# Optimization experiments

Hardware: AMD Instinct MI355X
Metric: run time of the kernel (lower is better)

The kernel has to match this reference:

```python
import jax, jax.numpy as jnp
import numpy as np

N = 10000
IN_DIM = 256
HID = 256
HEADS = 8
NUM_CLASSES = 40
EPS = 1e-5
NEG_SLOPE = 0.2


def gat_conv(x, src, dst, W, a_src, a_dst, bias, concat):
    # x: [N, F_in]; W: [F_in, H*C]; a_src/a_dst: [H, C]
    n = x.shape[0]
    H, C = a_src.shape
    h = (x @ W).reshape(n, H, C)                       # [N,H,C]
    s_src = jnp.einsum('nhc,hc->nh', h, a_src)         # [N,H]
    s_dst = jnp.einsum('nhc,hc->nh', h, a_dst)         # [N,H]
    score = jax.nn.leaky_relu(s_src[src] + s_dst[dst], NEG_SLOPE)  # [E,H]
    m = jax.lax.stop_gradient(jax.ops.segment_max(score, dst, num_segments=n))
    e = jnp.exp(score - m[dst])                        # [E,H]
    denom = jax.ops.segment_sum(e, dst, num_segments=n)
    alpha = e / denom[dst]                             # per-dst edge softmax
    msg = h[src] * alpha[:, :, None]                   # [E,H,C]
    out = jax.ops.segment_sum(msg, dst, num_segments=n)  # [N,H,C]
    out = out.reshape(n, H * C) if concat else out.mean(axis=1)
    return out + bias


def batch_norm(x, gamma, beta):
    mu = x.mean(axis=0)
    var = x.var(axis=0)
    return gamma * (x - mu) * jax.lax.rsqrt(var + EPS) + beta


def setup_inputs() -> dict:
    key = jax.random.key(0)
    ks = jax.random.split(key, 16)
    C0 = HID // HEADS  # 32, concat layer
    x = jax.random.normal(ks[0], (N, IN_DIM), jnp.float32)
    edge_index = jax.random.randint(ks[1], (2, 160000), 0, N, jnp.int32)
    def lin(k, fi, fo):
        return jax.random.normal(k, (fi, fo), jnp.float32) / np.sqrt(fi)
    return {
        'x': x,
        'edge_index': edge_index,
        'W0': lin(ks[2], IN_DIM, HEADS * C0),
        'a_src0': jax.random.normal(ks[3], (HEADS, C0), jnp.float32) * 0.1,
        'a_dst0': jax.random.normal(ks[4], (HEADS, C0), jnp.float32) * 0.1,
        'b0': jnp.zeros((HID,), jnp.float32),
        'g0': jnp.ones((HID,), jnp.float32),
        'be0': jnp.zeros((HID,), jnp.float32),
        'W1': lin(ks[5], HID, HEADS * HID),
        'a_src1': jax.random.normal(ks[6], (HEADS, HID), jnp.float32) * 0.1,
        'a_dst1': jax.random.normal(ks[7], (HEADS, HID), jnp.float32) * 0.1,
        'b1': jnp.zeros((HID,), jnp.float32),
        'g1': jnp.ones((HID,), jnp.float32),
        'be1': jnp.zeros((HID,), jnp.float32),
        'Wc': lin(ks[8], HID, NUM_CLASSES),
        'bc': jnp.zeros((NUM_CLASSES,), jnp.float32),
    }


def reference(x, edge_index, W0, a_src0, a_dst0, b0, g0, be0,
              W1, a_src1, a_dst1, b1, g1, be1, Wc, bc):
    n = x.shape[0]
    loops = jnp.arange(n, dtype=edge_index.dtype)
    src = jnp.concatenate([edge_index[0], loops])  # add_self_loops=True
    dst = jnp.concatenate([edge_index[1], loops])

    # layer 0: concat=True -> [N, 256]
    h = gat_conv(x, src, dst, W0, a_src0, a_dst0, b0, concat=True)
    h = jax.nn.elu(batch_norm(h, g0, be0))
    # i==0: no residual; dropout is identity at eval

    # layer 1 (last): concat=False (mean over heads) -> [N, 256]
    h_in = h
    h = gat_conv(h, src, dst, W1, a_src1, a_dst1, b1, concat=False)
    h = jax.nn.elu(batch_norm(h, g1, be1)) + h_in  # residual for i>0

    return h @ Wc + bc  # logits [N, num_classes]
```

## Files before the change

### kernel.cpp

```cpp
#include <hip/hip_runtime.h>
#include <math.h>

#define NN 10000
#define HEADS 8
#define NCLS 40
#define CHK 64
#define LOG2E 1.4426950408889634f

typedef __attribute__((ext_vector_type(8))) short short8;
typedef __attribute__((ext_vector_type(8))) unsigned short ushort8v;
typedef __attribute__((ext_vector_type(4))) float floatx4;

static __device__ __forceinline__ short f2bf(float f) {
    unsigned u = __builtin_bit_cast(unsigned, f);
    unsigned r = (u + 0x7fff + ((u >> 16) & 1)) >> 16;
    return (short)r;
}
static __device__ __forceinline__ float bf2f(unsigned short u) {
    unsigned x = ((unsigned)u) << 16;
    return __builtin_bit_cast(float, x);
}
static __device__ __forceinline__ void gl2lds16(const void* g, void* l) {
    __builtin_amdgcn_global_load_lds(
        (const __attribute__((address_space(1))) unsigned int*)g,
        (__attribute__((address_space(3))) unsigned int*)l, 16, 0, 0);
}

__global__ __launch_bounds__(256) void gemm_bf16_w128(
    const short* __restrict__ A, const short* __restrict__ Bt,
    float* __restrict__ C, short* __restrict__ Cbf,
    float* __restrict__ stats,
    const float* __restrict__ asrc, const float* __restrict__ adst,
    float* __restrict__ s0,
    const int* __restrict__ esrc, const int* __restrict__ edst,
    int* __restrict__ cursor, int* __restrict__ elist, int E, int scatBlocks,
    const float* __restrict__ W1, const float* __restrict__ a_src1,
    const float* __restrict__ a_dst1, float* __restrict__ v1,
    short* __restrict__ W1pT,
    int gemmBlocks, int gridY,
    int M, int Nn, int K, float alpha)
{
    __shared__ short As[64 * 64];
    __shared__ short Bs[128 * 64];
    const int tid = threadIdx.x;
    if ((int)blockIdx.x >= gemmBlocks) {
        int td = (int)blockIdx.x - gemmBlocks;
        if (td < scatBlocks) {
            int e = td * 256 + tid;
            if (e < E) {
                int dn = edst[e];
                int pos = atomicAdd(&cursor[dn], 1);
                elist[pos] = esrc[e];
            }
            return;
        }
        td -= scatBlocks;
        if (td < 16) {
            int idx = td * 256 + tid;
            int f = idx >> 4, j = idx & 15;
            int h = j & 7;
            const float* a = (j < 8) ? a_src1 : a_dst1;
            float s = 0.f;
            for (int c = 0; c < 256; c++)
                s += W1[f * 2048 + h * 256 + c] * a[h * 256 + c];
            v1[idx] = s;
            return;
        }
        td -= 16;
        {
            float (*tile)[33] = (float(*)[33])As;
            int h = td >> 6, f0 = ((td >> 3) & 7) * 32, c0 = (td & 7) * 32;
            int tx = tid & 31, ty = tid >> 5;
            for (int r = ty; r < 32; r += 8)
                tile[r][tx] = W1[(size_t)(f0 + r) * 2048 + h * 256 + c0 + tx];
            __syncthreads();
            for (int r = ty; r < 32; r += 8)
                W1pT[(size_t)(c0 + r) * 2048 + h * 256 + f0 + tx] = f2bf(tile[tx][r]);
            return;
        }
    }
    const int w = tid >> 6, L = tid & 63;
    const int quad = L >> 4, lr = L & 15;
    const int d = blockIdx.x;
    const int by = (d >> 4) * 8 + (d & 7);
    const int bx = (d >> 3) & 1;
    if (by >= gridY) return;
    const int col0 = bx * 128, row0 = by * 64;

    const int schunk = (L & 7) ^ (L >> 3);
    const int sarow = w * 16 + (L >> 3);
    int ga0 = row0 + sarow;     if (ga0 > M - 1) ga0 = M - 1;
    int ga1 = row0 + sarow + 8; if (ga1 > M - 1) ga1 = M - 1;
    const short* agp0 = A + (size_t)ga0 * K + schunk * 8;
    const short* agp1 = A + (size_t)ga1 * K + schunk * 8;
    short* alp0 = &As[w * 1024];
    short* alp1 = &As[w * 1024 + 512];
    const int sbrow = w * 32 + (L >> 3);
    int gb[4];
    #pragma unroll
    for (int c = 0; c < 4; c++) {
        gb[c] = col0 + sbrow + c * 8;
        if (gb[c] > Nn - 1) gb[c] = Nn - 1;
    }
    const short* bgp0 = Bt + (size_t)gb[0] * K + schunk * 8;
    const short* bgp1 = Bt + (size_t)gb[1] * K + schunk * 8;
    const short* bgp2 = Bt + (size_t)gb[2] * K + schunk * 8;
    const short* bgp3 = Bt + (size_t)gb[3] * K + schunk * 8;
    short* blp0 = &Bs[w * 2048];
    short* blp1 = &Bs[w * 2048 + 512];
    short* blp2 = &Bs[w * 2048 + 1024];
    short* blp3 = &Bs[w * 2048 + 1536];

    floatx4 acc[4][2];
    const floatx4 zf = {0.f, 0.f, 0.f, 0.f};
    #pragma unroll
    for (int i = 0; i < 4; i++)
        #pragma unroll
        for (int j = 0; j < 2; j++) acc[i][j] = zf;

    for (int k0 = 0; k0 < K; k0 += 64) {
        gl2lds16(agp0 + k0, alp0);
        gl2lds16(agp1 + k0, alp1);
        gl2lds16(bgp0 + k0, blp0);
        gl2lds16(bgp1 + k0, blp1);
        gl2lds16(bgp2 + k0, blp2);
        gl2lds16(bgp3 + k0, blp3);
        __syncthreads();
        #pragma unroll
        for (int ks = 0; ks < 2; ks++) {
            const int sl = ((ks * 4 + quad) ^ (lr & 7)) * 8;
            short8 bfr[2];
            #pragma unroll
            for (int j = 0; j < 2; j++)
                bfr[j] = *(const short8*)&Bs[(w * 32 + j * 16 + lr) * 64 + sl];
            #pragma unroll
            for (int i = 0; i < 4; i++) {
                short8 afr = *(const short8*)&As[(i * 16 + lr) * 64 + sl];
                #pragma unroll
                for (int j = 0; j < 2; j++)
                    acc[i][j] = __builtin_amdgcn_mfma_f32_16x16x32_bf16(afr, bfr[j], acc[i][j], 0, 0, 0);
            }
        }
        __syncthreads();
    }
    float s[2] = {0.f, 0.f}, s2[2] = {0.f, 0.f};
    #pragma unroll
    for (int j = 0; j < 2; j++) {
        int ccol = col0 + w * 32 + j * 16 + lr;
        if (ccol >= Nn) continue;
        #pragma unroll
        for (int i = 0; i < 4; i++) {
            #pragma unroll
            for (int r = 0; r < 4; r++) {
                int crow = row0 + i * 16 + quad * 4 + r;
                if (crow < M) {
                    float v = alpha * acc[i][j][r];
                    if (C)   C[(size_t)crow * Nn + ccol] = v;
                    if (Cbf) Cbf[(size_t)crow * Nn + ccol] = f2bf(v);
                    s[j] += v; s2[j] += v * v;
                }
            }
        }
    }
    if (stats) {
        #pragma unroll
        for (int j = 0; j < 2; j++) {
            s[j]  += __shfl_xor(s[j], 16, 64);  s[j]  += __shfl_xor(s[j], 32, 64);
            s2[j] += __shfl_xor(s2[j], 16, 64); s2[j] += __shfl_xor(s2[j], 32, 64);
        }
        if (L < 16) {
            #pragma unroll
            for (int j = 0; j < 2; j++) {
                int ccol = col0 + w * 32 + j * 16 + L;
                if (ccol < Nn) {
                    atomicAdd(&stats[ccol], s[j]);
                    atomicAdd(&stats[256 + ccol], s2[j]);
                }
            }
        }
    }
    if (s0) {
        const int head = bx * 4 + w;
        float as0 = asrc[col0 + w * 32 + lr];
        float as1 = asrc[col0 + w * 32 + 16 + lr];
        float ad0 = adst[col0 + w * 32 + lr];
        float ad1 = adst[col0 + w * 32 + 16 + lr];
        #pragma unroll
        for (int i = 0; i < 4; i++) {
            #pragma unroll
            for (int r = 0; r < 4; r++) {
                float ps = acc[i][0][r] * as0 + acc[i][1][r] * as1;
                float pd = acc[i][0][r] * ad0 + acc[i][1][r] * ad1;
                #pragma unroll
                for (int off = 1; off < 16; off <<= 1) {
                    ps += __shfl_xor(ps, off, 64);
                    pd += __shfl_xor(pd, off, 64);
                }
                if (lr == 0) {
                    int crow = row0 + i * 16 + quad * 4 + r;
                    if (crow < M) {
                        s0[crow * 16 + head] = alpha * ps;
                        s0[crow * 16 + 8 + head] = alpha * pd;
                    }
                }
            }
        }
    }
}

__global__ __launch_bounds__(256) void classifier_fused(
    const float* __restrict__ X, const float* __restrict__ stats,
    const float* __restrict__ g, const float* __restrict__ be,
    const unsigned short* __restrict__ resid,
    const short* __restrict__ Bt, float* __restrict__ C,
    const float* __restrict__ bias, int M, int Nn, int K)
{
    __shared__ short As[64 * 64];
    __shared__ short Bs[64 * 64];
    const int tid = threadIdx.x;
    const int w = tid >> 6, L = tid & 63;
    const int quad = L >> 4, lr = L & 15;
    const int row0 = blockIdx.x * 64;

    const int srow = w * 16 + (L >> 3);
    const int schunk = (L & 7) ^ (L >> 3);
    int ga0 = row0 + srow;     if (ga0 > M - 1)  ga0 = M - 1;
    int ga1 = row0 + srow + 8; if (ga1 > M - 1)  ga1 = M - 1;
    int gb0 = srow;     if (gb0 > Nn - 1) gb0 = Nn - 1;
    int gb1 = srow + 8; if (gb1 > Nn - 1) gb1 = Nn - 1;
    const float* xg0 = X + (size_t)ga0 * K + schunk * 8;
    const float* xg1 = X + (size_t)ga1 * K + schunk * 8;
    const unsigned short* rg0 = resid + (size_t)ga0 * K + schunk * 8;
    const unsigned short* rg1 = resid + (size_t)ga1 * K + schunk * 8;
    const short* bgp0 = Bt + (size_t)gb0 * K + schunk * 8;
    const short* bgp1 = Bt + (size_t)gb1 * K + schunk * 8;
    short* alw0 = &As[w * 1024 + L * 8];
    short* alw1 = &As[w * 1024 + 512 + L * 8];
    short* blp0 = &Bs[w * 1024];
    short* blp1 = &Bs[w * 1024 + 512];

    floatx4 acc[4];
    const floatx4 zf = {0.f, 0.f, 0.f, 0.f};
    #pragma unroll
    for (int i = 0; i < 4; i++) acc[i] = zf;
    const float invN = 1.0f / NN;

    for (int k0 = 0; k0 < K; k0 += 64) {
        gl2lds16(bgp0 + k0, blp0);
        gl2lds16(bgp1 + k0, blp1);
        const int c = schunk * 8 + k0;
        floatx4 mu_a = *(const floatx4*)(stats + c);
        floatx4 mu_b = *(const floatx4*)(stats + c + 4);
        floatx4 sq_a = *(const floatx4*)(stats + 256 + c);
        floatx4 sq_b = *(const floatx4*)(stats + 256 + c + 4);
        floatx4 g_a  = *(const floatx4*)(g + c);
        floatx4 g_b  = *(const floatx4*)(g + c + 4);
        floatx4 be_a = *(const floatx4*)(be + c);
        floatx4 be_b = *(const floatx4*)(be + c + 4);
        float scl[8], sh[8];
        #pragma unroll
        for (int q = 0; q < 8; q++) {
            float m  = (q < 4 ? mu_a[q & 3] : mu_b[q & 3]) * invN;
            float sq = (q < 4 ? sq_a[q & 3] : sq_b[q & 3]) * invN;
            float gv = (q < 4 ? g_a[q & 3]  : g_b[q & 3]);
            float bv = (q < 4 ? be_a[q & 3] : be_b[q & 3]);
            float rs = rsqrtf(sq - m * m + 1e-5f) * gv;
            scl[q] = rs; sh[q] = bv - m * rs;
        }
        {
            floatx4 xa = *(const floatx4*)(xg0 + k0);
            floatx4 xb2 = *(const floatx4*)(xg0 + k0 + 4);
            ushort8v rv = *(const ushort8v*)(rg0 + k0);
            short8 av;
            #pragma unroll
            for (int q = 0; q < 8; q++) {
                float v = (q < 4 ? xa[q & 3] : xb2[q & 3]) * scl[q] + sh[q];
                v = (v > 0.f) ? v : (expf(v) - 1.f);
                v += bf2f(rv[q]);
                av[q] = f2bf(v);
            }
            *(short8*)alw0 = av;
        }
        {
            floatx4 xa = *(const floatx4*)(xg1 + k0);
            floatx4 xb2 = *(const floatx4*)(xg1 + k0 + 4);
            ushort8v rv = *(const ushort8v*)(rg1 + k0);
            short8 av;
            #pragma unroll
            for (int q = 0; q < 8; q++) {
                float v = (q < 4 ? xa[q & 3] : xb2[q & 3]) * scl[q] + sh[q];
                v = (v > 0.f) ? v : (expf(v) - 1.f);
                v += bf2f(rv[q]);
                av[q] = f2bf(v);
            }
            *(short8*)alw1 = av;
        }
        __syncthreads();
        #pragma unroll
        for (int ks = 0; ks < 2; ks++) {
            const int sl = ((ks * 4 + quad) ^ (lr & 7)) * 8;
            short8 bfr = *(const short8*)&Bs[(w * 16 + lr) * 64 + sl];
            #pragma unroll
            for (int i = 0; i < 4; i++) {
                short8 afr = *(const short8*)&As[(i * 16 + lr) * 64 + sl];
                acc[i] = __builtin_amdgcn_mfma_f32_16x16x32_bf16(afr, bfr, acc[i], 0, 0, 0);
            }
        }
        __syncthreads();
    }
    const int ccol = w * 16 + lr;
    if (ccol < Nn) {
        float bv = bias ? bias[ccol] : 0.f;
        #pragma unroll
        for (int i = 0; i < 4; i++) {
            #pragma unroll
            for (int r = 0; r < 4; r++) {
                int crow = row0 + i * 16 + quad * 4 + r;
                if (crow < M) C[(size_t)crow * Nn + ccol] = acc[i][r] + bv;
            }
        }
    }
}

__global__ __launch_bounds__(256) void prep_a(
    const float* __restrict__ x, const float* __restrict__ W0,
    const float* __restrict__ Wc, const int* __restrict__ edst, int E,
    short* __restrict__ xb, short* __restrict__ W0T, short* __restrict__ WcT,
    int* __restrict__ counts)
{
    const int b = blockIdx.x, t = threadIdx.x;
    if (b < 2500) {
        int i = b * 256 + t;
        floatx4 v = ((const floatx4*)x)[i];
        short4 o = {f2bf(v[0]), f2bf(v[1]), f2bf(v[2]), f2bf(v[3])};
        ((short4*)xb)[i] = o;
    } else if (b < 2756) {
        int o = b - 2500;
        W0T[o * 256 + t] = f2bf(W0[t * 256 + o]);
    } else if (b < 2796) {
        int o = b - 2756;
        WcT[o * 256 + t] = f2bf(Wc[t * 40 + o]);
    } else {
        int e = (b - 2796) * 256 + t;
        if (e < E) atomicAdd(&counts[edst[e]], 1);
    }
}

__global__ __launch_bounds__(256) void scan_kernel(
    int* __restrict__ counts, int* __restrict__ offsets,
    int* __restrict__ cursor, int* __restrict__ elist, int n)
{
    __shared__ int wsum[4];
    const int t = threadIdx.x;
    const int P = (n + 255) >> 8;
    const int lane = t & 63, wid = t >> 6;
    const int base = t * P;
    int s = 0;
    for (int j = 0; j < P; j++) {
        int i = base + j;
        if (i < n) s += counts[i] + 1;
    }
    int inc = s;
    #pragma unroll
    for (int off = 1; off < 64; off <<= 1) {
        int tv = __shfl_up(inc, off, 64);
        if (lane >= off) inc += tv;
    }
    if (lane == 63) wsum[wid] = inc;
    __syncthreads();
    int wo = 0;
    #pragma unroll
    for (int k2 = 0; k2 < 4; k2++) {
        int v = wsum[k2];
        if (k2 < wid) wo += v;
    }
    int run = wo + inc - s;
    for (int j = 0; j < P; j++) {
        int i = base + j;
        if (i < n) {
            int d2 = counts[i] + 1;
            counts[i] = d2;
            offsets[i] = run;
            elist[run] = i;
            cursor[i] = run + 1;
            run += d2;
        }
    }
}

__global__ __launch_bounds__(256) void agg0_fused(
    const unsigned short* __restrict__ h0b, const float* __restrict__ s0,
    const int* __restrict__ offsets, const int* __restrict__ counts,
    const int* __restrict__ elist, float* __restrict__ out)
{
    __shared__ float pw_s[4][CHK * 8];
    __shared__ int   sn_s[4][CHK];
    const int wid = threadIdx.x >> 6, L = threadIdx.x & 63;
    const int n = blockIdx.x * 4 + wid;
    float* pw = pw_s[wid];
    int*   sw = sn_s[wid];
    const int deg = counts[n], start = offsets[n];
    const int hL = L >> 3;

    floatx4 sda = *(const floatx4*)(s0 + n * 16 + 8);
    floatx4 sdb = *(const floatx4*)(s0 + n * 16 + 12);
    float sd[8] = {sda[0], sda[1], sda[2], sda[3], sdb[0], sdb[1], sdb[2], sdb[3]};
    float lp[8] = {0.f, 0.f, 0.f, 0.f, 0.f, 0.f, 0.f, 0.f};
    float a0 = 0.f, a1 = 0.f, a2 = 0.f, a3 = 0.f;

    for (int e0 = 0; e0 < deg; e0 += CHK) {
        int ch = deg - e0; if (ch > CHK) ch = CHK;
        if (L < ch) {
            int sn = elist[start + e0 + L];
            sw[L] = sn;
            floatx4 ssa = *(const floatx4*)(s0 + sn * 16);
            floatx4 ssb = *(const floatx4*)(s0 + sn * 16 + 4);
            float ss[8] = {ssa[0], ssa[1], ssa[2], ssa[3], ssb[0], ssb[1], ssb[2], ssb[3]};
            float p[8];
            #pragma unroll
            for (int h = 0; h < 8; h++) {
                float v = ss[h] + sd[h];
                v = (v > 0.f) ? v : 0.2f * v;
                p[h] = exp2f(v * LOG2E);
                lp[h] += p[h];
            }
            floatx4 p0 = {p[0], p[1], p[2], p[3]};
            floatx4 p1 = {p[4], p[5], p[6], p[7]};
            *(floatx4*)&pw[L * 8] = p0;
            *(floatx4*)&pw[L * 8 + 4] = p1;
        }
        int e = 0;
        for (; e + 2 <= ch; e += 2) {
            float wA = pw[e * 8 + hL];
            float wB = pw[e * 8 + 8 + hL];
            ushort4 vA = *(const ushort4*)(h0b + (size_t)sw[e] * 256 + 4 * L);
            ushort4 vB = *(const ushort4*)(h0b + (size_t)sw[e + 1] * 256 + 4 * L);
            a0 += wA * bf2f(vA.x); a1 += wA * bf2f(vA.y);
            a2 += wA * bf2f(vA.z); a3 += wA * bf2f(vA.w);
            a0 += wB * bf2f(vB.x); a1 += wB * bf2f(vB.y);
            a2 += wB * bf2f(vB.z); a3 += wB * bf2f(vB.w);
        }
        if (e < ch) {
            float wA = pw[e * 8 + hL];
            ushort4 vA = *(const ushort4*)(h0b + (size_t)sw[e] * 256 + 4 * L);
            a0 += wA * bf2f(vA.x); a1 += wA * bf2f(vA.y);
            a2 += wA * bf2f(vA.z); a3 += wA * bf2f(vA.w);
        }
    }
    #pragma unroll
    for (int off = 1; off < 64; off <<= 1)
        #pragma unroll
        for (int h = 0; h < 8; h++)
            lp[h] += __shfl_xor(lp[h], off, 64);
    float inv = 1.f / lp[hL];
    floatx4 o = {a0 * inv, a1 * inv, a2 * inv, a3 * inv};
    *(floatx4*)(out + (size_t)n * 256 + 4 * L) = o;
}

__global__ __launch_bounds__(256) void agg1_full(
    const unsigned short* __restrict__ hb, const float* __restrict__ s1,
    const int* __restrict__ offsets, const int* __restrict__ counts,
    const int* __restrict__ elist, short* __restrict__ aggout)
{
    __shared__ float pw_s[4][CHK * 8];
    __shared__ int   sn_s[4][CHK];
    const int wid = threadIdx.x >> 6, L = threadIdx.x & 63;
    const int n = blockIdx.x * 4 + wid;
    float* pw = pw_s[wid];
    int*   sw = sn_s[wid];
    const int deg = counts[n], start = offsets[n];

    floatx4 sda = *(const floatx4*)(s1 + n * 16 + 8);
    floatx4 sdb = *(const floatx4*)(s1 + n * 16 + 12);
    float sd[8] = {sda[0], sda[1], sda[2], sda[3], sdb[0], sdb[1], sdb[2], sdb[3]};
    float lp[8] = {0.f, 0.f, 0.f, 0.f, 0.f, 0.f, 0.f, 0.f};
    float acc[8][4];
    #pragma unroll
    for (int h = 0; h < 8; h++)
        #pragma unroll
        for (int f = 0; f < 4; f++) acc[h][f] = 0.f;

    for (int e0 = 0; e0 < deg; e0 += CHK) {
        int ch = deg - e0; if (ch > CHK) ch = CHK;
        if (L < ch) {
            int sn = elist[start + e0 + L];
            sw[L] = sn;
            floatx4 ssa = *(const floatx4*)(s1 + sn * 16);
            floatx4 ssb = *(const floatx4*)(s1 + sn * 16 + 4);
            float ss[8] = {ssa[0], ssa[1], ssa[2], ssa[3], ssb[0], ssb[1], ssb[2], ssb[3]};
            float p[8];
            #pragma unroll
            for (int h = 0; h < 8; h++) {
                float v = ss[h] + sd[h];
                v = (v > 0.f) ? v : 0.2f * v;
                p[h] = exp2f(v * LOG2E);
                lp[h] += p[h];
            }
            floatx4 p0 = {p[0], p[1], p[2], p[3]};
            floatx4 p1 = {p[4], p[5], p[6], p[7]};
            *(floatx4*)&pw[L * 8] = p0;
            *(floatx4*)&pw[L * 8 + 4] = p1;
        }
        int e = 0;
        for (; e + 2 <= ch; e += 2) {
            floatx4 p0A = *(const floatx4*)&pw[e * 8];
            floatx4 p1A = *(const floatx4*)&pw[e * 8 + 4];
            floatx4 p0B = *(const floatx4*)&pw[e * 8 + 8];
            floatx4 p1B = *(const floatx4*)&pw[e * 8 + 12];
            ushort4 vA = *(const ushort4*)(hb + (size_t)sw[e] * 256 + 4 * L);
            ushort4 vB = *(const ushort4*)(hb + (size_t)sw[e + 1] * 256 + 4 * L);
            float a0 = bf2f(vA.x), a1 = bf2f(vA.y), a2 = bf2f(vA.z), a3 = bf2f(vA.w);
            float b0 = bf2f(vB.x), b1 = bf2f(vB.y), b2 = bf2f(vB.z), b3 = bf2f(vB.w);
            #pragma unroll
            for (int h = 0; h < 4; h++) {
                acc[h][0] += p0A[h] * a0;     acc[h][1] += p0A[h] * a1;
                acc[h][2] += p0A[h] * a2;     acc[h][3] += p0A[h] * a3;
                acc[h + 4][0] += p1A[h] * a0; acc[h + 4][1] += p1A[h] * a1;
                acc[h + 4][2] += p1A[h] * a2; acc[h + 4][3] += p1A[h] * a3;
            }
            #pragma unroll
            for (int h = 0; h < 4; h++) {
                acc[h][0] += p0B[h] * b0;     acc[h][1] += p0B[h] * b1;
                acc[h][2] += p0B[h] * b2;     acc[h][3] += p0B[h] * b3;
                acc[h + 4][0] += p1B[h] * b0; acc[h + 4][1] += p1B[h] * b1;
                acc[h + 4][2] += p1B[h] * b2; acc[h + 4][3] += p1B[h] * b3;
            }
        }
        if (e < ch) {
            floatx4 p0A = *(const floatx4*)&pw[e * 8];
            floatx4 p1A = *(const floatx4*)&pw[e * 8 + 4];
            ushort4 vA = *(const ushort4*)(hb + (size_t)sw[e] * 256 + 4 * L);
            float a0 = bf2f(vA.x), a1 = bf2f(vA.y), a2 = bf2f(vA.z), a3 = bf2f(vA.w);
            #pragma unroll
            for (int h = 0; h < 4; h++) {
                acc[h][0] += p0A[h] * a0;     acc[h][1] += p0A[h] * a1;
                acc[h][2] += p0A[h] * a2;     acc[h][3] += p0A[h] * a3;
                acc[h + 4][0] += p1A[h] * a0; acc[h + 4][1] += p1A[h] * a1;
                acc[h + 4][2] += p1A[h] * a2; acc[h + 4][3] += p1A[h] * a3;
            }
        }
    }
    #pragma unroll
    for (int off = 1; off < 64; off <<= 1)
        #pragma unroll
        for (int h = 0; h < 8; h++)
            lp[h] += __shfl_xor(lp[h], off, 64);
    #pragma unroll
    for (int h = 0; h < 8; h++) {
        float inv = 1.f / lp[h];
        short4 o = {f2bf(acc[h][0] * inv), f2bf(acc[h][1] * inv),
                    f2bf(acc[h][2] * inv), f2bf(acc[h][3] * inv)};
        *(short4*)(aggout + (size_t)n * 2048 + h * 256 + 4 * L) = o;
    }
}

__global__ __launch_bounds__(1024) void bn_stats_kernel(
    const float* __restrict__ x, float* __restrict__ stats, int n)
{
    __shared__ float red[16][512];
    const int t = threadIdx.x;
    const int sub = t >> 6, c4 = (t & 63) * 4;
    floatx4 s = {0.f, 0.f, 0.f, 0.f}, s2 = {0.f, 0.f, 0.f, 0.f};
    for (int r = blockIdx.x * 16 + sub; r < n; r += gridDim.x * 16) {
        floatx4 v = *(const floatx4*)(x + (size_t)r * 256 + c4);
        s += v; s2 += v * v;
    }
    #pragma unroll
    for (int k = 0; k < 4; k++) {
        red[sub][c4 + k] = s[k];
        red[sub][256 + c4 + k] = s2[k];
    }
    __syncthreads();
    if (t < 512) {
        float acc = 0.f;
        #pragma unroll
        for (int i = 0; i < 16; i++) acc += red[i][t];
        atomicAdd(&stats[t], acc);
    }
}

__global__ __launch_bounds__(256) void bnapply_score1(
    const float* __restrict__ xg, const float* __restrict__ stats,
    const float* __restrict__ g, const float* __restrict__ be,
    const float* __restrict__ v1, short* __restrict__ hactb, float* __restrict__ s1)
{
    __shared__ float row[256];
    __shared__ float part[16][17];
    const int n = blockIdx.x, t = threadIdx.x;
    const float invN = 1.0f / NN;
    float mu = stats[t] * invN;
    float var = stats[256 + t] * invN - mu * mu;
    float v = g[t] * (xg[(size_t)n * 256 + t] - mu) * rsqrtf(var + 1e-5f) + be[t];
    v = (v > 0.f) ? v : (expf(v) - 1.f);
    hactb[(size_t)n * 256 + t] = f2bf(v);
    row[t] = v;
    __syncthreads();
    int j = t & 15, f0 = t >> 4;
    float p = 0.f;
    #pragma unroll
    for (int k = 0; k < 16; k++)
        p += row[f0 * 16 + k] * v1[(f0 * 16 + k) * 16 + j];
    part[f0][j] = p;
    __syncthreads();
    if (t < 16) {
        float s = 0.f;
        #pragma unroll
        for (int k = 0; k < 16; k++) s += part[k][t];
        s1[n * 16 + t] = s;
    }
}

extern "C" void kernel_launch(void* const* d_in, const int* in_sizes, int n_in,
                              void* d_out, int out_size, void* d_ws, size_t ws_size,
                              hipStream_t stream) {
    const float* x      = (const float*)d_in[0];
    const int*   eidx   = (const int*)d_in[1];
    const float* W0     = (const float*)d_in[2];
    const float* a_src0 = (const float*)d_in[3];
    const float* a_dst0 = (const float*)d_in[4];
    const float* g0     = (const float*)d_in[6];
    const float* be0    = (const float*)d_in[7];
    const float* W1     = (const float*)d_in[8];
    const float* a_src1 = (const float*)d_in[9];
    const float* a_dst1 = (const float*)d_in[10];
    const float* g1     = (const float*)d_in[12];
    const float* be1    = (const float*)d_in[13];
    const float* Wc     = (const float*)d_in[14];
    const float* bc     = (const float*)d_in[15];
    float* out = (float*)d_out;

    const int E = in_sizes[1] / 2;
    const int* esrc = eidx;
    const int* edst = eidx + E;

    char* ws = (char*)d_ws;
    size_t off = 0;
    auto alloc = [&](size_t bytes) {
        void* p = ws + off;
        off += (bytes + 255) & ~(size_t)255;
        return p;
    };
    float* stats   = (float*)alloc(1024 * 4);
    int*   counts  = (int*)alloc(NN * 4);
    float* out1    = (float*)alloc((size_t)NN * 256 * 4);
    short* h0b     = (short*)alloc((size_t)NN * 256 * 2);
    short* xb      = (short*)alloc((size_t)NN * 256 * 2);
    float* s0      = (float*)alloc((size_t)NN * 16 * 4);
    float* s1      = (float*)alloc((size_t)NN * 16 * 4);
    float* v1      = (float*)alloc(4096 * 4);
    float* h_gat0  = (float*)alloc((size_t)NN * 256 * 4);
    short* hactb   = (short*)alloc((size_t)NN * 256 * 2);
    short* agg1bf  = (short*)alloc((size_t)NN * 2048 * 2);
    short* W0T     = (short*)alloc((size_t)256 * 256 * 2);
    short* W1pT    = (short*)alloc((size_t)256 * 2048 * 2);
    short* WcT     = (short*)alloc((size_t)64 * 256 * 2);
    int* offsets   = (int*)alloc((NN + 16) * 4);
    int* cursor    = (int*)alloc(NN * 4);
    int* elist     = (int*)alloc((size_t)(E + NN) * 4);

    float* stats0 = stats;
    float* stats1 = stats + 512;

    hipMemsetAsync(stats, 0, 1024 * 4 + NN * 4, stream);

    const int cntBlocks = (E + 255) / 256;

    prep_a<<<2796 + cntBlocks, 256, 0, stream>>>(
        x, W0, Wc, edst, E, xb, W0T, WcT, counts);

    scan_kernel<<<1, 256, 0, stream>>>(counts, offsets, cursor, elist, NN);

    const int gy = (NN + 63) / 64;
    const int gB = 16 * ((gy + 7) / 8);

    gemm_bf16_w128<<<gB + cntBlocks + 528, 256, 0, stream>>>(
        xb, W0T, nullptr, h0b, nullptr,
        a_src0, a_dst0, s0,
        esrc, edst, cursor, elist, E, cntBlocks,
        W1, a_src1, a_dst1, v1, W1pT,
        gB, gy, NN, 256, 256, 1.0f);

    agg0_fused<<<NN / 4, 256, 0, stream>>>(
        (const unsigned short*)h0b, s0, offsets, counts, elist, h_gat0);
    bn_stats_kernel<<<64, 1024, 0, stream>>>(h_gat0, stats0, NN);
    bnapply_score1<<<NN, 256, 0, stream>>>(h_gat0, stats0, g0, be0, v1, hactb, s1);

    agg1_full<<<NN / 4, 256, 0, stream>>>(
        (const unsigned short*)hactb, s1, offsets, counts, elist, agg1bf);
    gemm_bf16_w128<<<gB, 256, 0, stream>>>(
        agg1bf, W1pT, out1, nullptr, stats1,
        nullptr, nullptr, nullptr,
        nullptr, nullptr, nullptr, nullptr, 0, 0,
        nullptr, nullptr, nullptr, nullptr, nullptr,
        gB, gy, NN, 256, 2048, 0.125f);

    classifier_fused<<<gy, 256, 0, stream>>>(
        out1, stats1, g1, be1, (const unsigned short*)hactb,
        WcT, out, bc, NN, NCLS, 256);
}
```

Measured before the change: 275.6 us.

## Widen GEMM tile to full 256 columns with 512 threads; halve classifier row tile

The bf16 GEMM now uses 512-thread blocks that each cover 64 rows by all 256 output columns, so every A tile is loaded once instead of twice and the swizzled 2D block mapping goes away. The extra prologue blocks (edge scatter, v1 projection, W1 transpose) are resized for 512 threads. The classifier kernel switches to 32-row tiles, doubling its grid to improve occupancy across CUs. The wider GEMM tile uses more LDS and halves the GEMM block count (157 blocks), which may leave CUs underfilled.

```diff
diff --git a/kernel.cpp b/kernel.cpp
--- a/kernel.cpp
+++ b/kernel.cpp
@@ -26,7 +26,7 @@
         (__attribute__((address_space(3))) unsigned int*)l, 16, 0, 0);
 }
 
-__global__ __launch_bounds__(256) void gemm_bf16_w128(
+__global__ __launch_bounds__(512) void gemm_bf16_w256(
     const short* __restrict__ A, const short* __restrict__ Bt,
     float* __restrict__ C, short* __restrict__ Cbf,
     float* __restrict__ stats,
@@ -37,16 +37,15 @@
     const float* __restrict__ W1, const float* __restrict__ a_src1,
     const float* __restrict__ a_dst1, float* __restrict__ v1,
     short* __restrict__ W1pT,
-    int gemmBlocks, int gridY,
-    int M, int Nn, int K, float alpha)
+    int gemmBlocks, int M, int K, float alpha)
 {
     __shared__ short As[64 * 64];
-    __shared__ short Bs[128 * 64];
+    __shared__ short Bs[256 * 64];
     const int tid = threadIdx.x;
     if ((int)blockIdx.x >= gemmBlocks) {
         int td = (int)blockIdx.x - gemmBlocks;
         if (td < scatBlocks) {
-            int e = td * 256 + tid;
+            int e = td * 512 + tid;
             if (e < E) {
                 int dn = edst[e];
                 int pos = atomicAdd(&cursor[dn], 1);
@@ -55,8 +54,8 @@
             return;
         }
         td -= scatBlocks;
-        if (td < 16) {
-            int idx = td * 256 + tid;
+        if (td < 8) {
+            int idx = td * 512 + tid;
             int f = idx >> 4, j = idx & 15;
             int h = j & 7;
             const float* a = (j < 8) ? a_src1 : a_dst1;
@@ -66,46 +65,33 @@
             v1[idx] = s;
             return;
         }
-        td -= 16;
+        td -= 8;
         {
             float (*tile)[33] = (float(*)[33])As;
             int h = td >> 6, f0 = ((td >> 3) & 7) * 32, c0 = (td & 7) * 32;
             int tx = tid & 31, ty = tid >> 5;
-            for (int r = ty; r < 32; r += 8)
+            for (int r = ty; r < 32; r += 16)
                 tile[r][tx] = W1[(size_t)(f0 + r) * 2048 + h * 256 + c0 + tx];
             __syncthreads();
-            for (int r = ty; r < 32; r += 8)
+            for (int r = ty; r < 32; r += 16)
                 W1pT[(size_t)(c0 + r) * 2048 + h * 256 + f0 + tx] = f2bf(tile[tx][r]);
             return;
         }
     }
     const int w = tid >> 6, L = tid & 63;
     const int quad = L >> 4, lr = L & 15;
-    const int d = blockIdx.x;
-    const int by = (d >> 4) * 8 + (d & 7);
-    const int bx = (d >> 3) & 1;
-    if (by >= gridY) return;
-    const int col0 = bx * 128, row0 = by * 64;
+    const int row0 = blockIdx.x * 64;
 
     const int schunk = (L & 7) ^ (L >> 3);
-    const int sarow = w * 16 + (L >> 3);
-    int ga0 = row0 + sarow;     if (ga0 > M - 1) ga0 = M - 1;
-    int ga1 = row0 + sarow + 8; if (ga1 > M - 1) ga1 = M - 1;
-    const short* agp0 = A + (size_t)ga0 * K + schunk * 8;
-    const short* agp1 = A + (size_t)ga1 * K + schunk * 8;
-    short* alp0 = &As[w * 1024];
-    short* alp1 = &As[w * 1024 + 512];
+    const int sarow = w * 8 + (L >> 3);
+    int ga = row0 + sarow; if (ga > M - 1) ga = M - 1;
+    const short* agp = A + (size_t)ga * K + schunk * 8;
+    short* alp = &As[w * 512];
     const int sbrow = w * 32 + (L >> 3);
-    int gb[4];
-    #pragma unroll
-    for (int c = 0; c < 4; c++) {
-        gb[c] = col0 + sbrow + c * 8;
-        if (gb[c] > Nn - 1) gb[c] = Nn - 1;
-    }
-    const short* bgp0 = Bt + (size_t)gb[0] * K + schunk * 8;
-    const short* bgp1 = Bt + (size_t)gb[1] * K + schunk * 8;
-    const short* bgp2 = Bt + (size_t)gb[2] * K + schunk * 8;
-    const short* bgp3 = Bt + (size_t)gb[3] * K + schunk * 8;
+    const short* bgp0 = Bt + (size_t)(sbrow +  0) * K + schunk * 8;
+    const short* bgp1 = Bt + (size_t)(sbrow +  8) * K + schunk * 8;
+    const short* bgp2 = Bt + (size_t)(sbrow + 16) * K + schunk * 8;
+    const short* bgp3 = Bt + (size_t)(sbrow + 24) * K + schunk * 8;
     short* blp0 = &Bs[w * 2048];
     short* blp1 = &Bs[w * 2048 + 512];
     short* blp2 = &Bs[w * 2048 + 1024];
@@ -119,8 +105,7 @@
         for (int j = 0; j < 2; j++) acc[i][j] = zf;
 
     for (int k0 = 0; k0 < K; k0 += 64) {
-        gl2lds16(agp0 + k0, alp0);
-        gl2lds16(agp1 + k0, alp1);
+        gl2lds16(agp + k0, alp);
         gl2lds16(bgp0 + k0, blp0);
         gl2lds16(bgp1 + k0, blp1);
         gl2lds16(bgp2 + k0, blp2);
@@ -146,8 +131,7 @@
     float s[2] = {0.f, 0.f}, s2[2] = {0.f, 0.f};
     #pragma unroll
     for (int j = 0; j < 2; j++) {
-        int ccol = col0 + w * 32 + j * 16 + lr;
-        if (ccol >= Nn) continue;
+        int ccol = w * 32 + j * 16 + lr;
         #pragma unroll
         for (int i = 0; i < 4; i++) {
             #pragma unroll
@@ -155,8 +139,8 @@
                 int crow = row0 + i * 16 + quad * 4 + r;
                 if (crow < M) {
                     float v = alpha * acc[i][j][r];
-                    if (C)   C[(size_t)crow * Nn + ccol] = v;
-                    if (Cbf) Cbf[(size_t)crow * Nn + ccol] = f2bf(v);
+                    if (C)   C[(size_t)crow * 256 + ccol] = v;
+                    if (Cbf) Cbf[(size_t)crow * 256 + ccol] = f2bf(v);
                     s[j] += v; s2[j] += v * v;
                 }
             }
@@ -171,20 +155,17 @@
         if (L < 16) {
             #pragma unroll
             for (int j = 0; j < 2; j++) {
-                int ccol = col0 + w * 32 + j * 16 + L;
-                if (ccol < Nn) {
-                    atomicAdd(&stats[ccol], s[j]);
-                    atomicAdd(&stats[256 + ccol], s2[j]);
-                }
+                int ccol = w * 32 + j * 16 + L;
+                atomicAdd(&stats[ccol], s[j]);
+                atomicAdd(&stats[256 + ccol], s2[j]);
             }
         }
     }
     if (s0) {
-        const int head = bx * 4 + w;
-        float as0 = asrc[col0 + w * 32 + lr];
-        float as1 = asrc[col0 + w * 32 + 16 + lr];
-        float ad0 = adst[col0 + w * 32 + lr];
-        float ad1 = adst[col0 + w * 32 + 16 + lr];
+        float as0 = asrc[w * 32 + lr];
+        float as1 = asrc[w * 32 + 16 + lr];
+        float ad0 = adst[w * 32 + lr];
+        float ad1 = adst[w * 32 + 16 + lr];
         #pragma unroll
         for (int i = 0; i < 4; i++) {
             #pragma unroll
@@ -199,8 +180,8 @@
                 if (lr == 0) {
                     int crow = row0 + i * 16 + quad * 4 + r;
                     if (crow < M) {
-                        s0[crow * 16 + head] = alpha * ps;
-                        s0[crow * 16 + 8 + head] = alpha * pd;
+                        s0[crow * 16 + w] = alpha * ps;
+                        s0[crow * 16 + 8 + w] = alpha * pd;
                     }
                 }
             }
@@ -215,34 +196,29 @@
     const short* __restrict__ Bt, float* __restrict__ C,
     const float* __restrict__ bias, int M, int Nn, int K)
 {
-    __shared__ short As[64 * 64];
+    __shared__ short As[32 * 64];
     __shared__ short Bs[64 * 64];
     const int tid = threadIdx.x;
     const int w = tid >> 6, L = tid & 63;
     const int quad = L >> 4, lr = L & 15;
-    const int row0 = blockIdx.x * 64;
-
-    const int srow = w * 16 + (L >> 3);
+    const int row0 = blockIdx.x * 32;
+
     const int schunk = (L & 7) ^ (L >> 3);
-    int ga0 = row0 + srow;     if (ga0 > M - 1)  ga0 = M - 1;
-    int ga1 = row0 + srow + 8; if (ga1 > M - 1)  ga1 = M - 1;
-    int gb0 = srow;     if (gb0 > Nn - 1) gb0 = Nn - 1;
-    int gb1 = srow + 8; if (gb1 > Nn - 1) gb1 = Nn - 1;
-    const float* xg0 = X + (size_t)ga0 * K + schunk * 8;
-    const float* xg1 = X + (size_t)ga1 * K + schunk * 8;
-    const unsigned short* rg0 = resid + (size_t)ga0 * K + schunk * 8;
-    const unsigned short* rg1 = resid + (size_t)ga1 * K + schunk * 8;
+    int ga = row0 + w * 8 + (L >> 3); if (ga > M - 1) ga = M - 1;
+    int gbrow = w * 16 + (L >> 3);
+    int gb0 = gbrow;     if (gb0 > Nn - 1) gb0 = Nn - 1;
+    int gb1 = gbrow + 8; if (gb1 > Nn - 1) gb1 = Nn - 1;
+    const float* xg = X + (size_t)ga * K + schunk * 8;
+    const unsigned short* rg = resid + (size_t)ga * K + schunk * 8;
     const short* bgp0 = Bt + (size_t)gb0 * K + schunk * 8;
     const short* bgp1 = Bt + (size_t)gb1 * K + schunk * 8;
-    short* alw0 = &As[w * 1024 + L * 8];
-    short* alw1 = &As[w * 1024 + 512 + L * 8];
+    short* alw = &As[w * 512 + L * 8];
     short* blp0 = &Bs[w * 1024];
     short* blp1 = &Bs[w * 1024 + 512];
 
-    floatx4 acc[4];
+    floatx4 acc[2];
     const floatx4 zf = {0.f, 0.f, 0.f, 0.f};
-    #pragma unroll
-    for (int i = 0; i < 4; i++) acc[i] = zf;
+    acc[0] = zf; acc[1] = zf;
     const float invN = 1.0f / NN;
 
     for (int k0 = 0; k0 < K; k0 += 64) {
@@ -268,9 +244,9 @@
             scl[q] = rs; sh[q] = bv - m * rs;
         }
         {
-            floatx4 xa = *(const floatx4*)(xg0 + k0);
-            floatx4 xb2 = *(const floatx4*)(xg0 + k0 + 4);
-            ushort8v rv = *(const ushort8v*)(rg0 + k0);
+            floatx4 xa = *(const floatx4*)(xg + k0);
+            floatx4 xb2 = *(const floatx4*)(xg + k0 + 4);
+            ushort8v rv = *(const ushort8v*)(rg + k0);
             short8 av;
             #pragma unroll
             for (int q = 0; q < 8; q++) {
@@ -279,21 +255,7 @@
                 v += bf2f(rv[q]);
                 av[q] = f2bf(v);
             }
-            *(short8*)alw0 = av;
-        }
-        {
-            floatx4 xa = *(const floatx4*)(xg1 + k0);
-            floatx4 xb2 = *(const floatx4*)(xg1 + k0 + 4);
-            ushort8v rv = *(const ushort8v*)(rg1 + k0);
-            short8 av;
-            #pragma unroll
-            for (int q = 0; q < 8; q++) {
-                float v = (q < 4 ? xa[q & 3] : xb2[q & 3]) * scl[q] + sh[q];
-                v = (v > 0.f) ? v : (expf(v) - 1.f);
-                v += bf2f(rv[q]);
-                av[q] = f2bf(v);
-            }
-            *(short8*)alw1 = av;
+            *(short8*)alw = av;
         }
         __syncthreads();
         #pragma unroll
@@ -301,7 +263,7 @@
             const int sl = ((ks * 4 + quad) ^ (lr & 7)) * 8;
             short8 bfr = *(const short8*)&Bs[(w * 16 + lr) * 64 + sl];
             #pragma unroll
-            for (int i = 0; i < 4; i++) {
+            for (int i = 0; i < 2; i++) {
                 short8 afr = *(const short8*)&As[(i * 16 + lr) * 64 + sl];
                 acc[i] = __builtin_amdgcn_mfma_f32_16x16x32_bf16(afr, bfr, acc[i], 0, 0, 0);
             }
@@ -312,7 +274,7 @@
     if (ccol < Nn) {
         float bv = bias ? bias[ccol] : 0.f;
         #pragma unroll
-        for (int i = 0; i < 4; i++) {
+        for (int i = 0; i < 2; i++) {
             #pragma unroll
             for (int r = 0; r < 4; r++) {
                 int crow = row0 + i * 16 + quad * 4 + r;
@@ -664,6 +626,7 @@
     hipMemsetAsync(stats, 0, 1024 * 4 + NN * 4, stream);
 
     const int cntBlocks = (E + 255) / 256;
+    const int scat512   = (E + 511) / 512;
 
     prep_a<<<2796 + cntBlocks, 256, 0, stream>>>(
         x, W0, Wc, edst, E, xb, W0T, WcT, counts);
@@ -671,14 +634,13 @@
     scan_kernel<<<1, 256, 0, stream>>>(counts, offsets, cursor, elist, NN);
 
     const int gy = (NN + 63) / 64;
-    const int gB = 16 * ((gy + 7) / 8);
-
-    gemm_bf16_w128<<<gB + cntBlocks + 528, 256, 0, stream>>>(
+
+    gemm_bf16_w256<<<gy + scat512 + 8 + 512, 512, 0, stream>>>(
         xb, W0T, nullptr, h0b, nullptr,
         a_src0, a_dst0, s0,
-        esrc, edst, cursor, elist, E, cntBlocks,
+        esrc, edst, cursor, elist, E, scat512,
         W1, a_src1, a_dst1, v1, W1pT,
-        gB, gy, NN, 256, 256, 1.0f);
+        gy, NN, 256, 1.0f);
 
     agg0_fused<<<NN / 4, 256, 0, stream>>>(
         (const unsigned short*)h0b, s0, offsets, counts, elist, h_gat0);
@@ -687,14 +649,14 @@
 
     agg1_full<<<NN / 4, 256, 0, stream>>>(
         (const unsigned short*)hactb, s1, offsets, counts, elist, agg1bf);
-    gemm_bf16_w128<<<gB, 256, 0, stream>>>(
+    gemm_bf16_w256<<<gy, 512, 0, stream>>>(
         agg1bf, W1pT, out1, nullptr, stats1,
         nullptr, nullptr, nullptr,
         nullptr, nullptr, nullptr, nullptr, 0, 0,
         nullptr, nullptr, nullptr, nullptr, nullptr,
-        gB, gy, NN, 256, 2048, 0.125f);
-
-    classifier_fused<<<gy, 256, 0, stream>>>(
+        gy, NN, 2048, 0.125f);
+
+    classifier_fused<<<(NN + 31) / 32, 256, 0, stream>>>(
         out1, stats1, g1, be1, (const unsigned short*)hactb,
         WcT, out, bc, NN, NCLS, 256);
 }
```

Measured after the change: 286.5 us. +4.0%, slower.
